# Performance work log

Hardware: AMD Instinct MI355X
Metric: run time of the kernel (lower is better)

## Reference

```python
import jax, jax.numpy as jnp
import numpy as np

DT = 0.1
B_SZ = 8192
T_HIST = 20
LEN_PRED = 30
FEAT = 32
N_LAYERS = 3
# state transition for constant-acceleration model (matches self.F in torch)
F_MAT = np.array([[1.0, DT, DT * DT / 2], [0.0, 1.0, DT], [0.0, 0.0, 1.0]], dtype=np.float32)


def setup_inputs() -> dict:
    key = jax.random.key(0)
    ks = jax.random.split(key, 16)
    # random-walk trajectories as history observations
    hist = jnp.cumsum(jax.random.normal(ks[0], (B_SZ, T_HIST, 2), jnp.float32) * 0.5, axis=1)
    k_lin = 1.0 / np.sqrt(FEAT)
    k_in = 1.0 / np.sqrt(24)

    def u(k, shape, scale):
        return jax.random.uniform(k, shape, jnp.float32, -scale, scale)

    return {
        "hist": hist,
        "max_accel_x": jnp.ones((1,), jnp.float32) * 10.0,
        "max_accel_y": jnp.ones((1,), jnp.float32) * 20.0,
        "velocity_std_x": jnp.ones((1,), jnp.float32) * 10.0,
        "acceleration_std_x": jnp.ones((1,), jnp.float32) * 10.0,
        "R_x_": jnp.array([0.0448], jnp.float32),
        "R_y_": jnp.array([0.001], jnp.float32),
        "G_x": jnp.array([0.0059, 0.2981, 0.0393], jnp.float32),
        "G_y": jnp.array([0.0059, 0.2981, 0.0393], jnp.float32) / 5.0,
        "Win_W": u(ks[1], (FEAT, 24), k_in),
        "Win_b": u(ks[2], (FEAT,), k_in),
        "enc_Wih": u(ks[3], (N_LAYERS, 4 * FEAT, FEAT), k_lin),
        "enc_Whh": u(ks[4], (N_LAYERS, 4 * FEAT, FEAT), k_lin),
        "enc_bih": u(ks[5], (N_LAYERS, 4 * FEAT), k_lin),
        "enc_bhh": u(ks[6], (N_LAYERS, 4 * FEAT), k_lin),
        "dec_Wih": u(ks[7], (N_LAYERS, 4 * FEAT, FEAT), k_lin),
        "dec_Whh": u(ks[8], (N_LAYERS, 4 * FEAT, FEAT), k_lin),
        "dec_bih": u(ks[9], (N_LAYERS, 4 * FEAT), k_lin),
        "dec_bhh": u(ks[10], (N_LAYERS, 4 * FEAT), k_lin),
        "Wout_W": u(ks[11], (4, FEAT), k_lin),
        "Wout_b": u(ks[12], (4,), k_lin),
        "len_pred": LEN_PRED,
    }


def reference(hist, max_accel_x, max_accel_y, velocity_std_x, acceleration_std_x,
              R_x_, R_y_, G_x, G_y, Win_W, Win_b,
              enc_Wih, enc_Whh, enc_bih, enc_bhh,
              dec_Wih, dec_Whh, dec_bih, dec_bhh,
              Wout_W, Wout_b, len_pred):
    B = hist.shape[0]
    F = jnp.asarray(F_MAT)
    R_x = R_x_[0] * R_x_[0]
    R_y = R_y_[0] * R_y_[0]
    Z_x = hist[:, :, 0]
    Z_y = hist[:, :, 1]

    def lstm(x, h, c, Wih, Whh, bih, bhh):
        g = x @ Wih.T + bih + h @ Whh.T + bhh
        i, f, gg, o = jnp.split(g, 4, axis=1)
        c = jax.nn.sigmoid(f) * c + jax.nn.sigmoid(i) * jnp.tanh(gg)
        h = jax.nn.sigmoid(o) * jnp.tanh(c)
        return h, c

    def stack(XP, h, c, Wih, Whh, bih, bhh):
        x = jnp.tanh(XP @ Win_W.T + Win_b)
        hs, cs = [], []
        for j in range(N_LAYERS):
            hj, cj = lstm(x, h[j], c[j], Wih[j], Whh[j], bih[j], bhh[j])
            hs.append(hj)
            cs.append(cj)
            x = cj  # torch code feeds the fresh CELL state to the next layer
        return jnp.stack(hs), jnp.stack(cs)

    def kpred(X, P, Q):
        return X @ F.T, jnp.einsum('ij,bjk,lk->bil', F, P, F) + Q

    def kupdate(X, P, z, R):
        y = z - X[:, 0]                      # innovation (H picks component 0)
        S = P[:, 0, 0] + R                   # innovation covariance (scalar)
        K = P[:, :, 0] / S[:, None]          # Kalman gain (B,3)
        return X + y[:, None] * K, P - K[:, :, None] * P[:, 0:1, :]

    def kinit(z0):
        # torch always calls _kalman_init with is_x=True (default), so both
        # axes use R_x / velocity_std_x / acceleration_std_x
        X = jnp.zeros((B, 3), hist.dtype).at[:, 0].set(z0)
        d = jnp.stack([R_x, velocity_std_x[0] ** 2, acceleration_std_x[0] ** 2])
        P = jnp.zeros((B, 3, 3), hist.dtype).at[:, jnp.arange(3), jnp.arange(3)].set(d)
        return X, P

    Qx_e = jnp.outer(G_x * max_accel_x[0], G_x * max_accel_x[0])
    Qy_e = jnp.outer(G_y * max_accel_y[0], G_y * max_accel_y[0])

    Xx, Px = kinit(Z_x[:, 0])
    Xy, Py = kinit(Z_y[:, 0])
    h = jnp.zeros((N_LAYERS, B, FEAT), hist.dtype)
    c = jnp.zeros_like(h)

    def enc_step(carry, zs):
        Xx, Px, Xy, Py, h, c = carry
        zx, zy = zs
        XP = jnp.concatenate([Xx, Xy, Px.reshape(B, 9), Py.reshape(B, 9)], 1)
        h, c = stack(XP, h, c, enc_Wih, enc_Whh, enc_bih, enc_bhh)
        Xx, Px = kpred(Xx, Px, Qx_e)
        Xy, Py = kpred(Xy, Py, Qy_e)
        Xx, Px = kupdate(Xx, Px, zx, R_x)
        Xy, Py = kupdate(Xy, Py, zy, R_y)
        return (Xx, Px, Xy, Py, h, c), None

    carry, _ = jax.lax.scan(enc_step, (Xx, Px, Xy, Py, h, c),
                            (Z_x[:, 1:].T, Z_y[:, 1:].T))

    oxx = jnp.outer(G_x, G_x)
    oyy = jnp.outer(G_y, G_y)

    def dec_step(carry, _):
        Xx, Px, Xy, Py, h, c = carry
        XP = jnp.concatenate([Xx, Xy, Px.reshape(B, 9), Py.reshape(B, 9)], 1)
        h, c = stack(XP, h, c, dec_Wih, dec_Whh, dec_bih, dec_bhh)
        pred = c[-1] @ Wout_W.T + Wout_b  # (B,4): [u_x, u_y, std_x, std_y]
        Xx = Xx.at[:, 2].set(DT * pred[:, 0])  # X[:,2] = B*u
        Xy = Xy.at[:, 2].set(DT * pred[:, 1])
        Qx = (pred[:, 2] ** 2)[:, None, None] * oxx
        Qy = (pred[:, 3] ** 2)[:, None, None] * oyy
        Xx, Px = kpred(Xx, Px, Qx)
        Xy, Py = kpred(Xy, Py, Qy)
        out = jnp.stack([Xx[:, 0], Xy[:, 0],
                         jnp.sqrt(Px[:, 0, 0]), jnp.sqrt(Py[:, 0, 0]),
                         jnp.zeros(B, hist.dtype)], axis=1)  # (B,5)
        return (Xx, Px, Xy, Py, h, c), out

    carry, ys = jax.lax.scan(dec_step, carry, None, length=len_pred)
    return jnp.transpose(ys, (1, 0, 2))  # (B, len_pred, 5)
```

## Files before the change

kernel.cpp:

```cpp
#include <hip/hip_runtime.h>
#include <math.h>

#define DT   0.1f
#define HDT  0.005f
#define T_HIST 20
#define LEN_PRED 30

typedef __attribute__((ext_vector_type(8))) short bfrag8;
typedef __attribute__((ext_vector_type(4))) float f32x4;
typedef __attribute__((ext_vector_type(2))) unsigned int u32x2;

#define WS_FRAG   0u
#define WS_WIN    98304u
#define WS_WOUT   100352u
#define WS_BIAS   101376u

static __device__ __forceinline__ unsigned short f2bf(float x) {
    union { float f; unsigned int u; } v; v.f = x;
    unsigned int r = v.u + 0x7fffu + ((v.u >> 16) & 1u);
    return (unsigned short)(r >> 16);
}

static __device__ __forceinline__ unsigned int cvtpk(float lo, float hi) {
    unsigned int r;
    asm("v_cvt_pk_bf16_f32 %0, %1, %2" : "=v"(r) : "v"(lo), "v"(hi));
    return r;
}

__global__ void prep_kernel(const float* __restrict__ Win_W,
                            const float* __restrict__ eWih, const float* __restrict__ eWhh,
                            const float* __restrict__ ebih, const float* __restrict__ ebhh,
                            const float* __restrict__ dWih, const float* __restrict__ dWhh,
                            const float* __restrict__ dbih, const float* __restrict__ dbhh,
                            const float* __restrict__ Wout_W,
                            char* __restrict__ ws)
{
    int i = blockIdx.x * blockDim.x + threadIdx.x;
    if (i < 49152) {
        int fi = i >> 9, within = i & 511;
        int lane = within >> 3, jj = within & 7;
        int t = fi & 7, c = (fi >> 3) & 1;
        int pl = fi >> 4;
        int l = pl % 3, ph = pl / 3;
        int p = lane & 15, q2 = lane >> 4;
        int gate = p & 3;
        int feat = (t >> 1) * 8 + 2 * (p >> 2) + (t & 1);
        int row = gate * 32 + feat;
        int k = q2 * 8 + jj;
        const float* W = (c == 0) ? (ph ? dWih : eWih) : (ph ? dWhh : eWhh);
        ((unsigned short*)(ws + WS_FRAG))[i] = f2bf(W[l * 4096 + row * 32 + k]);
    } else if (i < 50176) {
        int i2 = i - 49152;
        int w = i2 >> 9, within = i2 & 511;
        int lane = within >> 3, jj = within & 7;
        int p = lane & 15, q2 = lane >> 4;
        int k = q2 * 8 + jj;
        float v = (k < 24) ? Win_W[(w * 16 + p) * 24 + k] : 0.f;
        ((unsigned short*)(ws + WS_WIN))[i2] = f2bf(v);
    } else if (i < 50688) {
        int i3 = i - 50176;
        int lane = i3 >> 3, jj = i3 & 7;
        int p = lane & 15, q2 = lane >> 4;
        float v = Wout_W[(p & 3) * 32 + q2 * 8 + jj];
        ((unsigned short*)(ws + WS_WOUT))[i3] = f2bf(v);
    } else if (i < 51456) {
        int b = i - 50688;
        int ph = b / 384, rem = b % 384;
        int l = rem >> 7, w2 = rem & 127;
        int col = w2 >> 2, r = w2 & 3;
        const float* bi = ph ? dbih : ebih;
        const float* bh = ph ? dbhh : ebhh;
        ((float*)(ws + WS_BIAS))[b] = bi[l * 128 + r * 32 + col] + bh[l * 128 + r * 32 + col];
    }
}

__launch_bounds__(256, 2)
__global__ void kalman_lstm_kernel(const float* __restrict__ hist,
                                   const float* __restrict__ max_ax, const float* __restrict__ max_ay,
                                   const float* __restrict__ vstd, const float* __restrict__ astd,
                                   const float* __restrict__ Rx_, const float* __restrict__ Ry_,
                                   const float* __restrict__ Gx, const float* __restrict__ Gy,
                                   const float* __restrict__ Win_W, const float* __restrict__ Win_b,
                                   const float* __restrict__ Wout_b,
                                   const char* __restrict__ ws, float* __restrict__ out)
{
    __shared__ __align__(16) unsigned int xchC[3][2][4][16][4];
    __shared__ __align__(16) unsigned int xchH[3][2][4][16][4];
    __shared__ __align__(16) unsigned int xenc[T_HIST - 1][4][16][4];

    const int tid  = threadIdx.x;
    const int wv   = tid >> 6;
    const int lane = tid & 63;
    const int q    = lane >> 4;
    const int m    = lane & 15;
    const int be   = blockIdx.x * 16 + m;
    const f32x4 zero4 = {0.f, 0.f, 0.f, 0.f};

    const bfrag8* fragp = (const bfrag8*)(ws + WS_FRAG);
    const f32x4*  biasp = (const f32x4*)(ws + WS_BIAS);

    bfrag8 fragA[3][2][2];
    f32x4  biasV[3][2];
    auto load_phase = [&](int ph) {
#pragma unroll
        for (int l = 0; l < 3; ++l) {
#pragma unroll
            for (int c = 0; c < 2; ++c)
#pragma unroll
                for (int j = 0; j < 2; ++j)
                    fragA[l][c][j] = fragp[(((ph * 3 + l) * 2 + c) * 8 + (2 * wv + j)) * 64 + lane];
#pragma unroll
            for (int j = 0; j < 2; ++j)
                biasV[l][j] = biasp[ph * 96 + l * 32 + (wv * 8 + 2 * q + j)];
        }
    };
    load_phase(0);

    const int w = (wv >= 2) ? (wv - 2) : 0;
    bfrag8 winF = ((const bfrag8*)(ws + WS_WIN))[w * 64 + lane];
    f32x4 winBv;
#pragma unroll
    for (int r = 0; r < 4; ++r) winBv[r] = Win_b[w * 16 + q * 4 + r];
    bfrag8 woutF = ((const bfrag8*)(ws + WS_WOUT))[lane];
    const float wb0 = Wout_b[0], wb1 = Wout_b[1], wb2 = Wout_b[2], wb3 = Wout_b[3];

    const float rx = Rx_[0] * Rx_[0], ry = Ry_[0] * Ry_[0];
    const float gX0 = Gx[0], gX1 = Gx[1], gX2 = Gx[2];
    const float gY0 = Gy[0], gY1 = Gy[1], gY2 = Gy[2];
    const float gx00 = gX0*gX0, gx01 = gX0*gX1, gx02 = gX0*gX2,
                gx11 = gX1*gX1, gx12 = gX1*gX2, gx22 = gX2*gX2;
    const float gy00 = gY0*gY0, gy01 = gY0*gY1, gy02 = gY0*gY2,
                gy11 = gY1*gY1, gy12 = gY1*gY2, gy22 = gY2*gY2;
    const float sx2 = max_ax[0] * max_ax[0], sy2 = max_ay[0] * max_ay[0];
    const float ex00 = gx00*sx2, ex01 = gx01*sx2, ex02 = gx02*sx2,
                ex11 = gx11*sx2, ex12 = gx12*sx2, ex22 = gx22*sx2;
    const float ey00 = gy00*sy2, ey01 = gy01*sy2, ey02 = gy02*sy2,
                ey11 = gy11*sy2, ey12 = gy12*sy2, ey22 = gy22*sy2;
    const float pv = vstd[0] * vstd[0], pa = astd[0] * astd[0];

    float Xx0 = hist[be * 40 + 0], Xx1 = 0.f, Xx2 = 0.f;
    float Xy0 = hist[be * 40 + 1], Xy1 = 0.f, Xy2 = 0.f;
    float Px00 = rx, Px01 = 0.f, Px02 = 0.f, Px11 = pv, Px12 = 0.f, Px22 = pa;
    float Py00 = rx, Py01 = 0.f, Py02 = 0.f, Py11 = pv, Py12 = 0.f, Py22 = pa;

    bfrag8 winAf[2], winPf[2];
    f32x4  winCb[2];
    float wpx[8], wpy[8], wqx[8], wqy[8];
    {
        auto applyA_col = [&](int k, float* col) {
            float in[24];
#pragma unroll
            for (int j = 0; j < 24; ++j) in[j] = (j == k) ? 1.f : 0.f;
            col[0] = in[0] + DT * in[1]; col[1] = in[1]; col[2] = 0.f;
            col[3] = in[3] + DT * in[4]; col[4] = in[4]; col[5] = 0.f;
#pragma unroll
            for (int b = 0; b < 2; ++b) {
                int o = 6 + b * 9;
                float M[3][3];
#pragma unroll
                for (int j = 0; j < 3; ++j) {
                    M[0][j] = in[o + j] + DT * in[o + 3 + j] + HDT * in[o + 6 + j];
                    M[1][j] = in[o + 3 + j] + DT * in[o + 6 + j];
                    M[2][j] = in[o + 6 + j];
                }
#pragma unroll
                for (int i = 0; i < 3; ++i) {
                    col[o + 3 * i + 0] = M[i][0] + DT * M[i][1] + HDT * M[i][2];
                    col[o + 3 * i + 1] = M[i][1] + DT * M[i][2];
                    col[o + 3 * i + 2] = M[i][2];
                }
            }
        };
        union { bfrag8 f; unsigned short s[8]; } ua, up;
#pragma unroll
        for (int t = 0; t < 2; ++t) {
            int feat = 8 * (m >> 2) + 4 * t + (m & 3);
            const float* wr = Win_W + feat * 24;
#pragma unroll
            for (int jj = 0; jj < 8; ++jj) {
                int k = q * 8 + jj;
                float va = 0.f, vp = 0.f;
                if (k < 24) {
                    float col[24];
                    applyA_col(k, col);
                    vp = wr[k];
#pragma unroll
                    for (int j = 0; j < 24; ++j) va += wr[j] * col[j];
                }
                ua.s[jj] = f2bf(va);
                up.s[jj] = f2bf(vp);
            }
            winAf[t] = ua.f;
            winPf[t] = up.f;
#pragma unroll
            for (int r = 0; r < 4; ++r) winCb[t][r] = Win_b[8 * q + 4 * t + r];
        }
#pragma unroll
        for (int e = 0; e < 8; ++e) {
            const float* wr = Win_W + (8 * q + e) * 24;
            wpx[e] = wr[0] * (HDT * DT) + wr[1] * (DT * DT) + wr[2] * DT;
            wpy[e] = wr[3] * (HDT * DT) + wr[4] * (DT * DT) + wr[5] * DT;
            float sx = 0.f, sy = 0.f;
#pragma unroll
            for (int i2 = 0; i2 < 3; ++i2)
#pragma unroll
                for (int j2 = 0; j2 < 3; ++j2) {
                    sx += wr[6 + 3 * i2 + j2]  * (Gx[i2] * Gx[j2]);
                    sy += wr[15 + 3 * i2 + j2] * (Gy[i2] * Gy[j2]);
                }
            wqx[e] = sx; wqy[e] = sy;
        }
    }

    float creg[3][2];
#pragma unroll
    for (int l = 0; l < 3; ++l) { creg[l][0] = 0.f; creg[l][1] = 0.f; }

    auto sig = [](float z) { return __builtin_amdgcn_rcpf(1.f + __expf(-z)); };
    auto th  = [](float z) { return fmaf(-2.f, __builtin_amdgcn_rcpf(__expf(2.f * z) + 1.f), 1.f); };

    auto kpred9 = [](float& X0, float& X1, float& X2,
                     float& P00, float& P01, float& P02, float& P11, float& P12, float& P22,
                     float Q00, float Q01, float Q02, float Q11, float Q12, float Q22) {
        X0 = X0 + DT * X1 + HDT * X2;
        X1 = X1 + DT * X2;
        float M00 = P00 + DT * P01 + HDT * P02;
        float M01 = P01 + DT * P11 + HDT * P12;
        float M02 = P02 + DT * P12 + HDT * P22;
        float M11 = P11 + DT * P12;
        float M12 = P12 + DT * P22;
        float M22 = P22;
        P00 = M00 + DT * M01 + HDT * M02 + Q00;
        P01 = M01 + DT * M02 + Q01;
        P02 = M02 + Q02;
        P11 = M11 + DT * M12 + Q11;
        P12 = M12 + Q12;
        P22 = M22 + Q22;
    };
    auto kupd9 = [](float& X0, float& X1, float& X2,
                    float& P00, float& P01, float& P02, float& P11, float& P12, float& P22,
                    float z, float R) {
        float y = z - X0;
        float Sinv = 1.0f / (P00 + R);
        float K0 = P00 * Sinv, K1 = P01 * Sinv, K2 = P02 * Sinv;
        X0 += y * K0; X1 += y * K1; X2 += y * K2;
        float p00 = P00, p01 = P01, p02 = P02;
        P00 = p00 - K0 * p00;
        P01 = p01 - K0 * p01;
        P02 = p02 - K0 * p02;
        P11 = P11 - K1 * p01;
        P12 = P12 - K1 * p02;
        P22 = P22 - K2 * p02;
    };
    auto kf_enc_step = [&](int s) {
        float zx = hist[be * 40 + s * 2], zy = hist[be * 40 + s * 2 + 1];
        kpred9(Xx0, Xx1, Xx2, Px00, Px01, Px02, Px11, Px12, Px22, ex00, ex01, ex02, ex11, ex12, ex22);
        kupd9 (Xx0, Xx1, Xx2, Px00, Px01, Px02, Px11, Px12, Px22, zx, rx);
        kpred9(Xy0, Xy1, Xy2, Py00, Py01, Py02, Py11, Py12, Py22, ey00, ey01, ey02, ey11, ey12, ey22);
        kupd9 (Xy0, Xy1, Xy2, Py00, Py01, Py02, Py11, Py12, Py22, zy, ry);
    };

    auto packf = [&](const float* v) {
        union { bfrag8 f; unsigned int u[4]; } u;
#pragma unroll
        for (int d = 0; d < 4; ++d) u.u[d] = cvtpk(v[2 * d], v[2 * d + 1]);
        return u.f;
    };
    auto build_xp = [&]() {
        float v[8];
        if (q == 0)      { v[0]=Xx0;  v[1]=Xx1;  v[2]=Xx2;  v[3]=Xy0;  v[4]=Xy1;  v[5]=Xy2;  v[6]=Px00; v[7]=Px01; }
        else if (q == 1) { v[0]=Px02; v[1]=Px01; v[2]=Px11; v[3]=Px12; v[4]=Px02; v[5]=Px12; v[6]=Px22; v[7]=Py00; }
        else if (q == 2) { v[0]=Py01; v[1]=Py02; v[2]=Py01; v[3]=Py11; v[4]=Py12; v[5]=Py02; v[6]=Py12; v[7]=Py22; }
        else             { v[0]=0.f; v[1]=0.f; v[2]=0.f; v[3]=0.f; v[4]=0.f; v[5]=0.f; v[6]=0.f; v[7]=0.f; }
        return packf(v);
    };

    auto gates_from = [&](int l, int j, f32x4 a, float& cv, float& hv) {
        float iv = sig(a[0]), fv = sig(a[1]), gv = th(a[2]), ov = sig(a[3]);
        float c = fmaf(fv, creg[l][j], iv * gv);
        creg[l][j] = c;
        cv = c;
        hv = ov * th(c);
    };

    for (int i = tid; i < 3 * 2 * 4 * 16 * 4; i += 256) {
        (&xchC[0][0][0][0][0])[i] = 0;
        (&xchH[0][0][0][0][0])[i] = 0;
    }

#pragma unroll 1
    for (int s = 0; s < T_HIST - 1; ++s) {
        if (s > 0) kf_enc_step(s);
        if (wv >= 2) {
            bfrag8 xpf = build_xp();
            f32x4 aw = __builtin_amdgcn_mfma_f32_16x16x32_bf16(winF, xpf, winBv, 0, 0, 0);
            u32x2 pk; pk.x = cvtpk(th(aw[0]), th(aw[1])); pk.y = cvtpk(th(aw[2]), th(aw[3]));
            *(u32x2*)&xenc[s][2 * w + (q >> 1)][m][(q & 1) * 2] = pk;
        }
    }
    kf_enc_step(T_HIST - 1);
    __syncthreads();

#pragma unroll 1
    for (int p = 0; p < T_HIST + 1; ++p) {
        const int pw = p & 1, pr = pw ^ 1;
        const bool b0 = (p <= T_HIST - 2);
        const bool b1 = (p >= 1) && (p <= T_HIST - 1);
        const bool b2 = (p >= 2);
        unsigned int cd0, hd0, cd1, hd1, cd2, hd2;
        if (b0) {
            bfrag8 xf = *(const bfrag8*)&xenc[p][q][m][0];
            bfrag8 hf = *(const bfrag8*)&xchH[0][pr][q][m][0];
            f32x4 a = __builtin_amdgcn_mfma_f32_16x16x32_bf16(fragA[0][1][0], hf, biasV[0][0], 0, 0, 0);
            a = __builtin_amdgcn_mfma_f32_16x16x32_bf16(fragA[0][0][0], xf, a, 0, 0, 0);
            f32x4 b = __builtin_amdgcn_mfma_f32_16x16x32_bf16(fragA[0][1][1], hf, biasV[0][1], 0, 0, 0);
            b = __builtin_amdgcn_mfma_f32_16x16x32_bf16(fragA[0][0][1], xf, b, 0, 0, 0);
            float c0, h0, c1, h1;
            gates_from(0, 0, a, c0, h0); gates_from(0, 1, b, c1, h1);
            cd0 = cvtpk(c0, c1); hd0 = cvtpk(h0, h1);
        }
        if (b1) {
            bfrag8 xf = *(const bfrag8*)&xchC[0][pr][q][m][0];
            bfrag8 hf = *(const bfrag8*)&xchH[1][pr][q][m][0];
            f32x4 a = __builtin_amdgcn_mfma_f32_16x16x32_bf16(fragA[1][1][0], hf, biasV[1][0], 0, 0, 0);
            a = __builtin_amdgcn_mfma_f32_16x16x32_bf16(fragA[1][0][0], xf, a, 0, 0, 0);
            f32x4 b = __builtin_amdgcn_mfma_f32_16x16x32_bf16(fragA[1][1][1], hf, biasV[1][1], 0, 0, 0);
            b = __builtin_amdgcn_mfma_f32_16x16x32_bf16(fragA[1][0][1], xf, b, 0, 0, 0);
            float c0, h0, c1, h1;
            gates_from(1, 0, a, c0, h0); gates_from(1, 1, b, c1, h1);
            cd1 = cvtpk(c0, c1); hd1 = cvtpk(h0, h1);
        }
        if (b2) {
            bfrag8 xf = *(const bfrag8*)&xchC[1][pr][q][m][0];
            bfrag8 hf = *(const bfrag8*)&xchH[2][pr][q][m][0];
            f32x4 a = __builtin_amdgcn_mfma_f32_16x16x32_bf16(fragA[2][1][0], hf, biasV[2][0], 0, 0, 0);
            a = __builtin_amdgcn_mfma_f32_16x16x32_bf16(fragA[2][0][0], xf, a, 0, 0, 0);
            f32x4 b = __builtin_amdgcn_mfma_f32_16x16x32_bf16(fragA[2][1][1], hf, biasV[2][1], 0, 0, 0);
            b = __builtin_amdgcn_mfma_f32_16x16x32_bf16(fragA[2][0][1], xf, b, 0, 0, 0);
            float c0, h0, c1, h1;
            gates_from(2, 0, a, c0, h0); gates_from(2, 1, b, c1, h1);
            cd2 = cvtpk(c0, c1); hd2 = cvtpk(h0, h1);
        }
        if (b0) { xchC[0][pw][wv][m][q] = cd0; xchH[0][pw][wv][m][q] = hd0; }
        if (b1) { xchC[1][pw][wv][m][q] = cd1; xchH[1][pw][wv][m][q] = hd1; }
        if (b2) { xchC[2][pw][wv][m][q] = cd2; xchH[2][pw][wv][m][q] = hd2; }
        __syncthreads();
    }

    load_phase(1);
    bfrag8 hfragR[3];
    hfragR[0] = *(const bfrag8*)&xchH[0][0][q][m][0];
    hfragR[1] = *(const bfrag8*)&xchH[1][1][q][m][0];
    hfragR[2] = *(const bfrag8*)&xchH[2][0][q][m][0];
    bfrag8 c2f = *(const bfrag8*)&xchC[2][0][q][m][0];

    bfrag8 xp = build_xp();
    f32x4 wp0 = __builtin_amdgcn_mfma_f32_16x16x32_bf16(winPf[0], xp, winCb[0], 0, 0, 0);
    f32x4 wp1 = __builtin_amdgcn_mfma_f32_16x16x32_bf16(winPf[1], xp, winCb[1], 0, 0, 0);
    __syncthreads();

    float px = 0.f, py = 0.f, qsx = 0.f, qsy = 0.f;
#pragma unroll 1
    for (int t = 0; t < LEN_PRED; ++t) {
        if (t > 0) {
            f32x4 ap = __builtin_amdgcn_mfma_f32_16x16x32_bf16(woutF, c2f, zero4, 0, 0, 0);
            px = ap[0] + wb0; py = ap[1] + wb1;
            float qe2 = ap[2] + wb2, qe3 = ap[3] + wb3;
            qsx = qe2 * qe2; qsy = qe3 * qe3;
        }
        float xv[8];
#pragma unroll
        for (int e = 0; e < 8; ++e) {
            float pre = (e < 4) ? wp0[e] : wp1[e - 4];
            xv[e] = th(fmaf(px, wpx[e], fmaf(py, wpy[e], fmaf(qsx, wqx[e], fmaf(qsy, wqy[e], pre)))));
        }
        bfrag8 xf = packf(xv);
        f32x4 ah[3][2];
#pragma unroll
        for (int l = 0; l < 3; ++l)
#pragma unroll
            for (int j = 0; j < 2; ++j)
                ah[l][j] = __builtin_amdgcn_mfma_f32_16x16x32_bf16(fragA[l][1][j], hfragR[l], biasV[l][j], 0, 0, 0);
        if (t > 0) {
            Xx2 = DT * px; Xy2 = DT * py;
            kpred9(Xx0, Xx1, Xx2, Px00, Px01, Px02, Px11, Px12, Px22,
                   qsx*gx00, qsx*gx01, qsx*gx02, qsx*gx11, qsx*gx12, qsx*gx22);
            kpred9(Xy0, Xy1, Xy2, Py00, Py01, Py02, Py11, Py12, Py22,
                   qsy*gy00, qsy*gy01, qsy*gy02, qsy*gy11, qsy*gy12, qsy*gy22);
            if (wv == 0 && q == 0) {
                float* o = out + (size_t)be * (LEN_PRED * 5) + (t - 1) * 5;
                o[0] = Xx0; o[1] = Xy0; o[2] = sqrtf(Px00); o[3] = sqrtf(Py00); o[4] = 0.f;
            }
        }
        xp = build_xp();
        wp0 = __builtin_amdgcn_mfma_f32_16x16x32_bf16(winAf[0], xp, winCb[0], 0, 0, 0);
        wp1 = __builtin_amdgcn_mfma_f32_16x16x32_bf16(winAf[1], xp, winCb[1], 0, 0, 0);
#pragma unroll
        for (int l = 0; l < 3; ++l) {
            f32x4 a0 = __builtin_amdgcn_mfma_f32_16x16x32_bf16(fragA[l][0][0], xf, ah[l][0], 0, 0, 0);
            f32x4 a1 = __builtin_amdgcn_mfma_f32_16x16x32_bf16(fragA[l][0][1], xf, ah[l][1], 0, 0, 0);
            float c0, h0, c1, h1;
            gates_from(l, 0, a0, c0, h0);
            gates_from(l, 1, a1, c1, h1);
            xchC[l][0][wv][m][q] = cvtpk(c0, c1);
            xchH[l][0][wv][m][q] = cvtpk(h0, h1);
            __syncthreads();
            xf        = *(const bfrag8*)&xchC[l][0][q][m][0];
            hfragR[l] = *(const bfrag8*)&xchH[l][0][q][m][0];
        }
        c2f = xf;
    }
    {
        f32x4 ap = __builtin_amdgcn_mfma_f32_16x16x32_bf16(woutF, c2f, zero4, 0, 0, 0);
        px = ap[0] + wb0; py = ap[1] + wb1;
        float qe2 = ap[2] + wb2, qe3 = ap[3] + wb3;
        qsx = qe2 * qe2; qsy = qe3 * qe3;
        Xx2 = DT * px; Xy2 = DT * py;
        kpred9(Xx0, Xx1, Xx2, Px00, Px01, Px02, Px11, Px12, Px22,
               qsx*gx00, qsx*gx01, qsx*gx02, qsx*gx11, qsx*gx12, qsx*gx22);
        kpred9(Xy0, Xy1, Xy2, Py00, Py01, Py02, Py11, Py12, Py22,
               qsy*gy00, qsy*gy01, qsy*gy02, qsy*gy11, qsy*gy12, qsy*gy22);
        if (wv == 0 && q == 0) {
            float* o = out + (size_t)be * (LEN_PRED * 5) + (LEN_PRED - 1) * 5;
            o[0] = Xx0; o[1] = Xy0; o[2] = sqrtf(Px00); o[3] = sqrtf(Py00); o[4] = 0.f;
        }
    }
}

extern "C" void kernel_launch(void* const* d_in, const int* in_sizes, int n_in,
                              void* d_out, int out_size, void* d_ws, size_t ws_size,
                              hipStream_t stream)
{
    const float* hist  = (const float*)d_in[0];
    const float* maxax = (const float*)d_in[1];
    const float* maxay = (const float*)d_in[2];
    const float* vstd  = (const float*)d_in[3];
    const float* astd  = (const float*)d_in[4];
    const float* Rx    = (const float*)d_in[5];
    const float* Ry    = (const float*)d_in[6];
    const float* Gx    = (const float*)d_in[7];
    const float* Gy    = (const float*)d_in[8];
    const float* WinW  = (const float*)d_in[9];
    const float* Winb  = (const float*)d_in[10];
    const float* eWih  = (const float*)d_in[11];
    const float* eWhh  = (const float*)d_in[12];
    const float* ebih  = (const float*)d_in[13];
    const float* ebhh  = (const float*)d_in[14];
    const float* dWih  = (const float*)d_in[15];
    const float* dWhh  = (const float*)d_in[16];
    const float* dbih  = (const float*)d_in[17];
    const float* dbhh  = (const float*)d_in[18];
    const float* WoutW = (const float*)d_in[19];
    const float* Woutb = (const float*)d_in[20];
    char* ws = (char*)d_ws;
    float* out = (float*)d_out;

    prep_kernel<<<202, 256, 0, stream>>>(WinW, eWih, eWhh, ebih, ebhh,
                                         dWih, dWhh, dbih, dbhh, WoutW, ws);
    kalman_lstm_kernel<<<512, 256, 0, stream>>>(hist, maxax, maxay, vstd, astd,
                                                Rx, Ry, Gx, Gy, WinW, Winb, Woutb,
                                                ws, out);
}
```

Before: 218.4 us.

## Precompute decoder input-projection fragments in prep kernel and apply pred correction via MFMA

Moves the per-block computation of the transition-folded Win fragments (winA, winP) and the per-feature pred coefficient vectors into the prep kernel, so every main-kernel block loads them from workspace instead of rebuilding them with scalar loops. In the decoder loop, the per-step scalar FMA correction for px/py/qsx/qsy is replaced by an extra pair of MFMAs against a packed bf16 coefficient fragment. This cuts prologue work and register pressure (32 float coefficient registers removed), at the cost of rounding the pred inputs and coefficients to bf16 and adding two MFMAs to the serial decoder chain.

```diff
diff --git a/kernel.cpp b/kernel.cpp
--- a/kernel.cpp
+++ b/kernel.cpp
@@ -14,6 +14,9 @@
 #define WS_WIN    98304u
 #define WS_WOUT   100352u
 #define WS_BIAS   101376u
+#define WS_WINP   104448u
+#define WS_WINA   106496u
+#define WS_WR4    108544u
 
 static __device__ __forceinline__ unsigned short f2bf(float x) {
     union { float f; unsigned int u; } v; v.f = x;
@@ -25,6 +28,31 @@
     unsigned int r;
     asm("v_cvt_pk_bf16_f32 %0, %1, %2" : "=v"(r) : "v"(lo), "v"(hi));
     return r;
+}
+
+static __device__ void applyA_col(int k, float* col) {
+    float in[24];
+#pragma unroll
+    for (int j = 0; j < 24; ++j) in[j] = (j == k) ? 1.f : 0.f;
+    col[0] = in[0] + DT * in[1]; col[1] = in[1]; col[2] = 0.f;
+    col[3] = in[3] + DT * in[4]; col[4] = in[4]; col[5] = 0.f;
+#pragma unroll
+    for (int b = 0; b < 2; ++b) {
+        int o = 6 + b * 9;
+        float M[3][3];
+#pragma unroll
+        for (int j = 0; j < 3; ++j) {
+            M[0][j] = in[o + j] + DT * in[o + 3 + j] + HDT * in[o + 6 + j];
+            M[1][j] = in[o + 3 + j] + DT * in[o + 6 + j];
+            M[2][j] = in[o + 6 + j];
+        }
+#pragma unroll
+        for (int i = 0; i < 3; ++i) {
+            col[o + 3 * i + 0] = M[i][0] + DT * M[i][1] + HDT * M[i][2];
+            col[o + 3 * i + 1] = M[i][1] + DT * M[i][2];
+            col[o + 3 * i + 2] = M[i][2];
+        }
+    }
 }
 
 __global__ void prep_kernel(const float* __restrict__ Win_W,
@@ -33,6 +61,7 @@
                             const float* __restrict__ dWih, const float* __restrict__ dWhh,
                             const float* __restrict__ dbih, const float* __restrict__ dbhh,
                             const float* __restrict__ Wout_W,
+                            const float* __restrict__ Gx, const float* __restrict__ Gy,
                             char* __restrict__ ws)
 {
     int i = blockIdx.x * blockDim.x + threadIdx.x;
@@ -71,6 +100,54 @@
         const float* bi = ph ? dbih : ebih;
         const float* bh = ph ? dbhh : ebhh;
         ((float*)(ws + WS_BIAS))[b] = bi[l * 128 + r * 32 + col] + bh[l * 128 + r * 32 + col];
+    } else if (i < 52480) {
+        int i4 = i - 51456;
+        int t = i4 >> 9, within = i4 & 511;
+        int lane = within >> 3, jj = within & 7;
+        int p = lane & 15, q2 = lane >> 4;
+        int feat = 8 * (p >> 2) + 4 * t + (p & 3);
+        int k = q2 * 8 + jj;
+        float v = (k < 24) ? Win_W[feat * 24 + k] : 0.f;
+        ((unsigned short*)(ws + WS_WINP))[i4] = f2bf(v);
+    } else if (i < 53504) {
+        int i5 = i - 52480;
+        int t = i5 >> 9, within = i5 & 511;
+        int lane = within >> 3, jj = within & 7;
+        int p = lane & 15, q2 = lane >> 4;
+        int feat = 8 * (p >> 2) + 4 * t + (p & 3);
+        int k = q2 * 8 + jj;
+        float v = 0.f;
+        if (k < 24) {
+            float col[24];
+            applyA_col(k, col);
+            const float* wr = Win_W + feat * 24;
+#pragma unroll
+            for (int j = 0; j < 24; ++j) v += wr[j] * col[j];
+        }
+        ((unsigned short*)(ws + WS_WINA))[i5] = f2bf(v);
+    } else if (i < 54528) {
+        int i6 = i - 53504;
+        int t = i6 >> 9, within = i6 & 511;
+        int lane = within >> 3, jj = within & 7;
+        int p = lane & 15, q2 = lane >> 4;
+        int feat = 8 * (p >> 2) + 4 * t + (p & 3);
+        int k = q2 * 8 + jj;
+        const float* wr = Win_W + feat * 24;
+        float v = 0.f;
+        if (k == 0)      v = wr[0] * (HDT * DT) + wr[1] * (DT * DT) + wr[2] * DT;
+        else if (k == 1) v = wr[3] * (HDT * DT) + wr[4] * (DT * DT) + wr[5] * DT;
+        else if (k == 2) {
+#pragma unroll
+            for (int a = 0; a < 3; ++a)
+#pragma unroll
+                for (int b = 0; b < 3; ++b) v += wr[6 + 3 * a + b] * Gx[a] * Gx[b];
+        } else if (k == 3) {
+#pragma unroll
+            for (int a = 0; a < 3; ++a)
+#pragma unroll
+                for (int b = 0; b < 3; ++b) v += wr[15 + 3 * a + b] * Gy[a] * Gy[b];
+        }
+        ((unsigned short*)(ws + WS_WR4))[i6] = f2bf(v);
     }
 }
 
@@ -80,8 +157,7 @@
                                    const float* __restrict__ vstd, const float* __restrict__ astd,
                                    const float* __restrict__ Rx_, const float* __restrict__ Ry_,
                                    const float* __restrict__ Gx, const float* __restrict__ Gy,
-                                   const float* __restrict__ Win_W, const float* __restrict__ Win_b,
-                                   const float* __restrict__ Wout_b,
+                                   const float* __restrict__ Win_b, const float* __restrict__ Wout_b,
                                    const char* __restrict__ ws, float* __restrict__ out)
 {
     __shared__ __align__(16) unsigned int xchC[3][2][4][16][4];
@@ -123,6 +199,16 @@
     for (int r = 0; r < 4; ++r) winBv[r] = Win_b[w * 16 + q * 4 + r];
     bfrag8 woutF = ((const bfrag8*)(ws + WS_WOUT))[lane];
     const float wb0 = Wout_b[0], wb1 = Wout_b[1], wb2 = Wout_b[2], wb3 = Wout_b[3];
+
+    bfrag8 winAf0 = ((const bfrag8*)(ws + WS_WINA))[lane];
+    bfrag8 winAf1 = ((const bfrag8*)(ws + WS_WINA))[64 + lane];
+    bfrag8 winR0  = ((const bfrag8*)(ws + WS_WR4))[lane];
+    bfrag8 winR1  = ((const bfrag8*)(ws + WS_WR4))[64 + lane];
+    f32x4 winCb[2];
+#pragma unroll
+    for (int t = 0; t < 2; ++t)
+#pragma unroll
+        for (int r = 0; r < 4; ++r) winCb[t][r] = Win_b[8 * q + 4 * t + r];
 
     const float rx = Rx_[0] * Rx_[0], ry = Ry_[0] * Ry_[0];
     const float gX0 = Gx[0], gX1 = Gx[1], gX2 = Gx[2];
@@ -142,75 +228,6 @@
     float Xy0 = hist[be * 40 + 1], Xy1 = 0.f, Xy2 = 0.f;
     float Px00 = rx, Px01 = 0.f, Px02 = 0.f, Px11 = pv, Px12 = 0.f, Px22 = pa;
     float Py00 = rx, Py01 = 0.f, Py02 = 0.f, Py11 = pv, Py12 = 0.f, Py22 = pa;
-
-    bfrag8 winAf[2], winPf[2];
-    f32x4  winCb[2];
-    float wpx[8], wpy[8], wqx[8], wqy[8];
-    {
-        auto applyA_col = [&](int k, float* col) {
-            float in[24];
-#pragma unroll
-            for (int j = 0; j < 24; ++j) in[j] = (j == k) ? 1.f : 0.f;
-            col[0] = in[0] + DT * in[1]; col[1] = in[1]; col[2] = 0.f;
-            col[3] = in[3] + DT * in[4]; col[4] = in[4]; col[5] = 0.f;
-#pragma unroll
-            for (int b = 0; b < 2; ++b) {
-                int o = 6 + b * 9;
-                float M[3][3];
-#pragma unroll
-                for (int j = 0; j < 3; ++j) {
-                    M[0][j] = in[o + j] + DT * in[o + 3 + j] + HDT * in[o + 6 + j];
-                    M[1][j] = in[o + 3 + j] + DT * in[o + 6 + j];
-                    M[2][j] = in[o + 6 + j];
-                }
-#pragma unroll
-                for (int i = 0; i < 3; ++i) {
-                    col[o + 3 * i + 0] = M[i][0] + DT * M[i][1] + HDT * M[i][2];
-                    col[o + 3 * i + 1] = M[i][1] + DT * M[i][2];
-                    col[o + 3 * i + 2] = M[i][2];
-                }
-            }
-        };
-        union { bfrag8 f; unsigned short s[8]; } ua, up;
-#pragma unroll
-        for (int t = 0; t < 2; ++t) {
-            int feat = 8 * (m >> 2) + 4 * t + (m & 3);
-            const float* wr = Win_W + feat * 24;
-#pragma unroll
-            for (int jj = 0; jj < 8; ++jj) {
-                int k = q * 8 + jj;
-                float va = 0.f, vp = 0.f;
-                if (k < 24) {
-                    float col[24];
-                    applyA_col(k, col);
-                    vp = wr[k];
-#pragma unroll
-                    for (int j = 0; j < 24; ++j) va += wr[j] * col[j];
-                }
-                ua.s[jj] = f2bf(va);
-                up.s[jj] = f2bf(vp);
-            }
-            winAf[t] = ua.f;
-            winPf[t] = up.f;
-#pragma unroll
-            for (int r = 0; r < 4; ++r) winCb[t][r] = Win_b[8 * q + 4 * t + r];
-        }
-#pragma unroll
-        for (int e = 0; e < 8; ++e) {
-            const float* wr = Win_W + (8 * q + e) * 24;
-            wpx[e] = wr[0] * (HDT * DT) + wr[1] * (DT * DT) + wr[2] * DT;
-            wpy[e] = wr[3] * (HDT * DT) + wr[4] * (DT * DT) + wr[5] * DT;
-            float sx = 0.f, sy = 0.f;
-#pragma unroll
-            for (int i2 = 0; i2 < 3; ++i2)
-#pragma unroll
-                for (int j2 = 0; j2 < 3; ++j2) {
-                    sx += wr[6 + 3 * i2 + j2]  * (Gx[i2] * Gx[j2]);
-                    sy += wr[15 + 3 * i2 + j2] * (Gy[i2] * Gy[j2]);
-                }
-            wqx[e] = sx; wqy[e] = sy;
-        }
-    }
 
     float creg[3][2];
 #pragma unroll
@@ -354,9 +371,14 @@
     hfragR[2] = *(const bfrag8*)&xchH[2][0][q][m][0];
     bfrag8 c2f = *(const bfrag8*)&xchC[2][0][q][m][0];
 
-    bfrag8 xp = build_xp();
-    f32x4 wp0 = __builtin_amdgcn_mfma_f32_16x16x32_bf16(winPf[0], xp, winCb[0], 0, 0, 0);
-    f32x4 wp1 = __builtin_amdgcn_mfma_f32_16x16x32_bf16(winPf[1], xp, winCb[1], 0, 0, 0);
+    f32x4 wp0, wp1;
+    {
+        bfrag8 winPf0 = ((const bfrag8*)(ws + WS_WINP))[lane];
+        bfrag8 winPf1 = ((const bfrag8*)(ws + WS_WINP))[64 + lane];
+        bfrag8 xp = build_xp();
+        wp0 = __builtin_amdgcn_mfma_f32_16x16x32_bf16(winPf0, xp, winCb[0], 0, 0, 0);
+        wp1 = __builtin_amdgcn_mfma_f32_16x16x32_bf16(winPf1, xp, winCb[1], 0, 0, 0);
+    }
     __syncthreads();
 
     float px = 0.f, py = 0.f, qsx = 0.f, qsy = 0.f;
@@ -368,12 +390,20 @@
             float qe2 = ap[2] + wb2, qe3 = ap[3] + wb3;
             qsx = qe2 * qe2; qsy = qe3 * qe3;
         }
+        bfrag8 uf;
+        {
+            union { bfrag8 f; unsigned int u[4]; } uu;
+            uu.u[0] = (q == 0) ? cvtpk(px, py) : 0u;
+            uu.u[1] = (q == 0) ? cvtpk(qsx, qsy) : 0u;
+            uu.u[2] = 0u; uu.u[3] = 0u;
+            uf = uu.f;
+        }
+        f32x4 x0a = __builtin_amdgcn_mfma_f32_16x16x32_bf16(winR0, uf, wp0, 0, 0, 0);
+        f32x4 x0b = __builtin_amdgcn_mfma_f32_16x16x32_bf16(winR1, uf, wp1, 0, 0, 0);
         float xv[8];
 #pragma unroll
-        for (int e = 0; e < 8; ++e) {
-            float pre = (e < 4) ? wp0[e] : wp1[e - 4];
-            xv[e] = th(fmaf(px, wpx[e], fmaf(py, wpy[e], fmaf(qsx, wqx[e], fmaf(qsy, wqy[e], pre)))));
-        }
+        for (int e = 0; e < 8; ++e)
+            xv[e] = th((e < 4) ? x0a[e] : x0b[e - 4]);
         bfrag8 xf = packf(xv);
         f32x4 ah[3][2];
 #pragma unroll
@@ -392,9 +422,11 @@
                 o[0] = Xx0; o[1] = Xy0; o[2] = sqrtf(Px00); o[3] = sqrtf(Py00); o[4] = 0.f;
             }
         }
-        xp = build_xp();
-        wp0 = __builtin_amdgcn_mfma_f32_16x16x32_bf16(winAf[0], xp, winCb[0], 0, 0, 0);
-        wp1 = __builtin_amdgcn_mfma_f32_16x16x32_bf16(winAf[1], xp, winCb[1], 0, 0, 0);
+        {
+            bfrag8 xp = build_xp();
+            wp0 = __builtin_amdgcn_mfma_f32_16x16x32_bf16(winAf0, xp, winCb[0], 0, 0, 0);
+            wp1 = __builtin_amdgcn_mfma_f32_16x16x32_bf16(winAf1, xp, winCb[1], 0, 0, 0);
+        }
 #pragma unroll
         for (int l = 0; l < 3; ++l) {
             f32x4 a0 = __builtin_amdgcn_mfma_f32_16x16x32_bf16(fragA[l][0][0], xf, ah[l][0], 0, 0, 0);
@@ -455,9 +487,10 @@
     char* ws = (char*)d_ws;
     float* out = (float*)d_out;
 
-    prep_kernel<<<202, 256, 0, stream>>>(WinW, eWih, eWhh, ebih, ebhh,
-                                         dWih, dWhh, dbih, dbhh, WoutW, ws);
+    prep_kernel<<<213, 256, 0, stream>>>(WinW, eWih, eWhh, ebih, ebhh,
+                                         dWih, dWhh, dbih, dbhh, WoutW,
+                                         Gx, Gy, ws);
     kalman_lstm_kernel<<<512, 256, 0, stream>>>(hist, maxax, maxay, vstd, astd,
-                                                Rx, Ry, Gx, Gy, WinW, Winb, Woutb,
+                                                Rx, Ry, Gx, Gy, Winb, Woutb,
                                                 ws, out);
 }
```

Result: faster. 192.2 us (-12.0%).
